# Optimization experiments

Measured on AMD Instinct MI355X. Metric: run time of the kernel, lower is better.

Reference implementation:

```python
import jax, jax.numpy as jnp
import numpy as np
import math

HID = 512
HEADS = 8
DK = HID // HEADS
B, S, T = 8, 4096, 512


def setup_inputs() -> dict:
    key = jax.random.key(0)
    ks = jax.random.split(key, 12)
    scale = 0.02
    inp = {
        "inputs": jax.random.normal(ks[0], (B, S, HID), dtype=jnp.float32),
        "targets": jax.random.normal(ks[1], (B, T, HID), dtype=jnp.float32),
        "mask": jnp.ones((B, S), dtype=bool),
        "Wq": jax.random.normal(ks[2], (HID, HID), dtype=jnp.float32) * scale,
        "bq": jnp.zeros((HID,), dtype=jnp.float32),
        "Wk": jax.random.normal(ks[3], (HID, HID), dtype=jnp.float32) * scale,
        "bk": jnp.zeros((HID,), dtype=jnp.float32),
        "Wv": jax.random.normal(ks[4], (HID, HID), dtype=jnp.float32) * scale,
        "bv": jnp.zeros((HID,), dtype=jnp.float32),
        "Wo": jax.random.normal(ks[5], (HID, HID), dtype=jnp.float32) * scale,
        "bo": jnp.zeros((HID,), dtype=jnp.float32),
    }
    return inp


def reference(inputs, targets, mask, Wq, bq, Wk, bk, Wv, bv, Wo, bo):
    # PoolingFunction(method='multihead-attention'), dropout=0 (identity),
    # hidden_size == output_size so mapping_function is identity.
    b, t, h = targets.shape
    s = inputs.shape[1]
    Q = (targets @ Wq.T + bq).reshape(b, t, HEADS, DK)
    K = (inputs @ Wk.T + bk).reshape(b, s, HEADS, DK)
    V = (inputs @ Wv.T + bv).reshape(b, s, HEADS, DK)
    # scores: b x heads x tgt x seq (same math as (Q*K).sum(-1)/sqrt(d_k))
    e = jnp.einsum('bthd,bshd->bhts', Q, K) / math.sqrt(DK)
    neg = (1.0 - mask.astype(jnp.float32)) * -1e20  # b x s
    e = e + neg[:, None, None, :]
    a = jax.nn.softmax(e, axis=-1)  # softmax over seq dim
    ctx = jnp.einsum('bhts,bshd->bthd', a, V).reshape(b, t, h)
    return ctx @ Wo.T + bo
```

## Files before the change

kernel.cpp:

```cpp
#include <hip/hip_runtime.h>
#include <hip/hip_bf16.h>
#include <cstdint>
#include <cstddef>

#define HIDN   512
#define NHEADS 8
#define BATCH  8
#define SLEN   4096
#define TLEN   512
#define SSPLIT 4
#define SCHUNK (SLEN / SSPLIT)
#define SCL2   0.18033688f

typedef __attribute__((ext_vector_type(8))) short   bf16x8;
typedef __attribute__((ext_vector_type(4))) float   f32x4;
typedef unsigned short u16;
typedef unsigned int   u32;

__device__ __forceinline__ u32 pkbf(float a, float b) {
    __hip_bfloat162 h = __float22bfloat162_rn(float2{a, b});
    union { __hip_bfloat162 h; u32 u; } un; un.h = h; return un.u;
}
__device__ __forceinline__ u32 cvtpk(float a, float b) {
    u32 r;
    asm("v_cvt_pk_bf16_f32 %0, %1, %2" : "=v"(r) : "v"(a), "v"(b));
    return r;
}
__device__ __forceinline__ float fexp2(float x) {
    return __builtin_amdgcn_exp2f(x);
}
__device__ __forceinline__ void gload_lds16(const u16* g, u16* l) {
    __builtin_amdgcn_global_load_lds(
        (const __attribute__((address_space(1))) u32*)g,
        (__attribute__((address_space(3))) u32*)l, 16, 0, 0);
}

__global__ __launch_bounds__(256) void cvt_all(
    const float* __restrict__ X, const float* __restrict__ Tg,
    const float* __restrict__ Wq, const float* __restrict__ Wk,
    const float* __restrict__ Wv, const float* __restrict__ Wo,
    const int* __restrict__ mask,
    u16* __restrict__ Xc, u16* __restrict__ Tc, u16* __restrict__ Wc,
    float* __restrict__ negf)
{
    int i4 = blockIdx.x * 256 + threadIdx.x;
    if (i4 >= 4980736) {
        int off = i4 - 4980736;
        int4 mv = ((const int4*)mask)[off];
        float4 nv;
        nv.x = mv.x ? 0.f : -1e30f; nv.y = mv.y ? 0.f : -1e30f;
        nv.z = mv.z ? 0.f : -1e30f; nv.w = mv.w ? 0.f : -1e30f;
        ((float4*)negf)[off] = nv;
        return;
    }
    const float* s; u16* d; long off;
    if (i4 < 4194304)      { s = X;  d = Xc; off = i4; }
    else if (i4 < 4718592) { s = Tg; d = Tc; off = i4 - 4194304; }
    else {
        int wi = i4 - 4718592; int widx = wi >> 16;
        s = (widx == 0) ? Wq : (widx == 1) ? Wk : (widx == 2) ? Wv : Wo;
        d = Wc + widx * 262144; off = wi & 65535;
    }
    float4 v = *(const float4*)(s + off * 4);
    uint2 o; o.x = pkbf(v.x, v.y); o.y = pkbf(v.z, v.w);
    *(uint2*)(d + off * 4) = o;
}

template<int MODE, int SEQ>
__global__ __launch_bounds__(256)
void gemm_bf16(const u16* __restrict__ A, const u16* __restrict__ Bw,
               const float* __restrict__ bias, void* __restrict__ Yv)
{
    __shared__ u16 As[128 * 32];
    __shared__ u16 Bs[128 * 32];
    const int tid = threadIdx.x;
    const int lane = tid & 63, w = tid >> 6;
    const int m = lane & 15, qd = lane >> 4;
    const int wm = w >> 1, wn = w & 1;
    const int m0 = blockIdx.y * 128, n0 = blockIdx.x * 128;

    f32x4 acc[4][4];
#pragma unroll
    for (int i = 0; i < 4; ++i)
#pragma unroll
        for (int j = 0; j < 4; ++j) acc[i][j] = (f32x4){0.f, 0.f, 0.f, 0.f};

    for (int k0 = 0; k0 < HIDN; k0 += 32) {
#pragma unroll
        for (int r = 0; r < 2; ++r) {
            const int f = tid + r * 256;
            const int row = f >> 2, c8 = (f & 3) * 8;
            const int fb = f & ~63;
            gload_lds16(A  + (size_t)(m0 + row) * HIDN + k0 + c8, As + fb * 8);
            gload_lds16(Bw + (size_t)(n0 + row) * HIDN + k0 + c8, Bs + fb * 8);
        }
        __syncthreads();
        bf16x8 af[4], bf[4];
#pragma unroll
        for (int t = 0; t < 4; ++t) {
            af[t] = *(bf16x8*)&As[(64 * wm + 16 * t + m) * 32 + 8 * qd];
            bf[t] = *(bf16x8*)&Bs[(64 * wn + 16 * t + m) * 32 + 8 * qd];
        }
#pragma unroll
        for (int ti = 0; ti < 4; ++ti)
#pragma unroll
            for (int tj = 0; tj < 4; ++tj)
                acc[ti][tj] = __builtin_amdgcn_mfma_f32_16x16x32_bf16(
                    af[ti], bf[tj], acc[ti][tj], 0, 0, 0);
        __syncthreads();
    }

#pragma unroll
    for (int ti = 0; ti < 4; ++ti) {
        const int gr0 = m0 + 64 * wm + 16 * ti + 4 * qd;
#pragma unroll
        for (int tj = 0; tj < 4; ++tj) {
            const int gcol = n0 + 64 * wn + 16 * tj + m;
            const float bv = bias[gcol];
            if (MODE == 0) {
                float* Y = (float*)Yv;
#pragma unroll
                for (int i = 0; i < 4; ++i)
                    Y[(size_t)(gr0 + i) * HIDN + gcol] = acc[ti][tj][i] + bv;
            } else {
                u16* Y = (u16*)Yv;
                const int b = gr0 / SEQ, h = gcol >> 6, d = gcol & 63;
                const int r = gr0 & (SEQ - 1);
                uint2 o;
                o.x = pkbf(acc[ti][tj][0] + bv, acc[ti][tj][1] + bv);
                o.y = pkbf(acc[ti][tj][2] + bv, acc[ti][tj][3] + bv);
                *(uint2*)&Y[(((size_t)(b * 8 + h)) * 64 + d) * SEQ + r] = o;
            }
        }
    }
}

template<int SEQ>
__global__ __launch_bounds__(256)
void gemm_wxT(const u16* __restrict__ Wm, const u16* __restrict__ X,
              const float* __restrict__ bias, u16* __restrict__ Y)
{
    __shared__ u16 As[128 * 32];
    __shared__ u16 Bs[128 * 32];
    const int tid = threadIdx.x;
    const int lane = tid & 63, w = tid >> 6;
    const int m = lane & 15, qd = lane >> 4;
    const int wm = w >> 1, wn = w & 1;
    const int m0 = blockIdx.y * 128, n0 = blockIdx.x * 128;

    f32x4 acc[4][4];
#pragma unroll
    for (int i = 0; i < 4; ++i)
#pragma unroll
        for (int j = 0; j < 4; ++j) acc[i][j] = (f32x4){0.f, 0.f, 0.f, 0.f};

    for (int k0 = 0; k0 < HIDN; k0 += 32) {
#pragma unroll
        for (int r = 0; r < 2; ++r) {
            const int f = tid + r * 256;
            const int row = f >> 2, c8 = (f & 3) * 8;
            const int fb = f & ~63;
            gload_lds16(Wm + (size_t)(m0 + row) * HIDN + k0 + c8, As + fb * 8);
            gload_lds16(X  + (size_t)(n0 + row) * HIDN + k0 + c8, Bs + fb * 8);
        }
        __syncthreads();
        bf16x8 af[4], bf[4];
#pragma unroll
        for (int t = 0; t < 4; ++t) {
            af[t] = *(bf16x8*)&As[(64 * wm + 16 * t + m) * 32 + 8 * qd];
            bf[t] = *(bf16x8*)&Bs[(64 * wn + 16 * t + m) * 32 + 8 * qd];
        }
#pragma unroll
        for (int ti = 0; ti < 4; ++ti)
#pragma unroll
            for (int tj = 0; tj < 4; ++tj)
                acc[ti][tj] = __builtin_amdgcn_mfma_f32_16x16x32_bf16(
                    af[ti], bf[tj], acc[ti][tj], 0, 0, 0);
        __syncthreads();
    }

#pragma unroll
    for (int ti = 0; ti < 4; ++ti) {
        const int o = m0 + 64 * wm + 16 * ti + 4 * qd;
        const float4 bv = *(const float4*)&bias[o];
        const int h = o >> 6, d0 = o & 63;
#pragma unroll
        for (int tj = 0; tj < 4; ++tj) {
            const int n = n0 + 64 * wn + 16 * tj + m;
            const int b = n / SEQ, r = n & (SEQ - 1);
            uint2 pk;
            pk.x = pkbf(acc[ti][tj][0] + bv.x, acc[ti][tj][1] + bv.y);
            pk.y = pkbf(acc[ti][tj][2] + bv.z, acc[ti][tj][3] + bv.w);
            *(uint2*)&Y[(((size_t)(b * 8 + h)) * SEQ + r) * 64 + d0] = pk;
        }
    }
}

__global__ __launch_bounds__(256, 2)
void attn_part(const u16* __restrict__ Q, const u16* __restrict__ K,
               const u16* __restrict__ Vt, const float* __restrict__ negf,
               float* __restrict__ Opart, float* __restrict__ lpart)
{
    __shared__ char Psh[32768];
    __shared__ u16  KVl[2][8192];
    __shared__ float Ngl[1024];
    const int tid = threadIdx.x;
    const int lane = tid & 63, w = tid >> 6;
    const int m = lane & 15, qd = lane >> 4;
    const int ti = blockIdx.x, si = blockIdx.y, bh = blockIdx.z;
    const int b = bh >> 3;

    const u16* Qp = Q + ((size_t)bh * TLEN + ti * 256) * 64;
    const u16* Kp = K + (size_t)bh * SLEN * 64;
    const u16* Vp = Vt + (size_t)bh * 64 * SLEN;
    const float* np = negf + (size_t)b * SLEN;
    const int s_beg = si * SCHUNK;

    const int sr = tid >> 3;
    const int sg = ((tid & 7) ^ (sr & 7)) * 8;
    const u16* kgb = Kp + (size_t)s_beg * 64 + sr * 64 + sg;
    const u16* vgb = Vp + s_beg + (size_t)sr * SLEN + sg;
    u16* kd = &KVl[0][0]    + tid * 8;
    u16* vd = &KVl[0][4096] + tid * 8;

#define STAGE(cc, bb) do {                                                   \
        const u16* kg_ = kgb + (size_t)(cc) * 4096;                          \
        const u16* vg_ = vgb + (cc) * 64;                                    \
        u16* kd_ = kd + (bb) * 8192;                                         \
        u16* vd_ = vd + (bb) * 8192;                                         \
        gload_lds16(kg_,                     kd_);                           \
        gload_lds16(kg_ + 32 * 64,           kd_ + 2048);                    \
        gload_lds16(vg_,                     vd_);                           \
        gload_lds16(vg_ + (size_t)32 * SLEN, vd_ + 2048);                    \
    } while (0)

    const int wb = w * 8192 + m * 128;
    int waddr[4], ra0[2], ra1[2];
#pragma unroll
    for (int st = 0; st < 4; ++st) waddr[st] = wb + (((4 * st + qd) ^ m) << 3);
#pragma unroll
    for (int ks = 0; ks < 2; ++ks) {
        const int u0 = 8 * ks + 2 * qd;
        ra0[ks] = wb + (((u0) ^ m) << 3);
        ra1[ks] = wb + (((u0 + 1) ^ m) << 3);
    }
    const int x0 = ((qd    ) ^ (m & 7)) * 8;
    const int x1 = ((4 + qd) ^ (m & 7)) * 8;

    bf16x8 qf[4][2];
#pragma unroll
    for (int ts = 0; ts < 4; ++ts)
#pragma unroll
        for (int kh = 0; kh < 2; ++kh)
            qf[ts][kh] = *(const bf16x8*)(Qp + (64 * w + 16 * ts + m) * 64 +
                                          32 * kh + 8 * qd);

    f32x4 O[4][4];
#pragma unroll
    for (int ts = 0; ts < 4; ++ts)
#pragma unroll
        for (int dt = 0; dt < 4; ++dt) O[ts][dt] = (f32x4){0.f, 0.f, 0.f, 0.f};
    float lr[4] = {0.f, 0.f, 0.f, 0.f};

#define CHUNK(cc) do {                                                       \
        const u16* Kl = &KVl[(cc) & 1][0];                                   \
        const u16* Vl = &KVl[(cc) & 1][4096];                                \
        bf16x8 kf[4][2];                                                     \
        _Pragma("unroll")                                                    \
        for (int st = 0; st < 4; ++st) {                                     \
            kf[st][0] = *(const bf16x8*)&Kl[st * 1024 + m * 64 + x0];        \
            kf[st][1] = *(const bf16x8*)&Kl[st * 1024 + m * 64 + x1];        \
        }                                                                    \
        float4 ng[4];                                                        \
        _Pragma("unroll")                                                    \
        for (int st = 0; st < 4; ++st)                                       \
            ng[st] = *(const float4*)&Ngl[((cc) << 6) + (st << 4) + (qd << 2)]; \
        _Pragma("unroll")                                                    \
        for (int ts = 0; ts < 4; ++ts) {                                     \
            f32x4 S[4];                                                      \
            _Pragma("unroll")                                                \
            for (int st = 0; st < 4; ++st) {                                 \
                f32x4 cc2 = (f32x4){0.f, 0.f, 0.f, 0.f};                     \
                cc2 = __builtin_amdgcn_mfma_f32_16x16x32_bf16(               \
                          kf[st][0], qf[ts][0], cc2, 0, 0, 0);               \
                cc2 = __builtin_amdgcn_mfma_f32_16x16x32_bf16(               \
                          kf[st][1], qf[ts][1], cc2, 0, 0, 0);               \
                S[st] = cc2;                                                 \
            }                                                                \
            float ls = 0.f;                                                  \
            _Pragma("unroll")                                                \
            for (int st = 0; st < 4; ++st) {                                 \
                const float p0 = fexp2(fmaf(S[st][0], SCL2, ng[st].x));      \
                const float p1 = fexp2(fmaf(S[st][1], SCL2, ng[st].y));      \
                const float p2 = fexp2(fmaf(S[st][2], SCL2, ng[st].z));      \
                const float p3 = fexp2(fmaf(S[st][3], SCL2, ng[st].w));      \
                ls += (p0 + p1) + (p2 + p3);                                 \
                *(uint2*)&Psh[waddr[st] + ts * 2048] =                       \
                    make_uint2(cvtpk(p0, p1), cvtpk(p2, p3));                \
            }                                                                \
            lr[ts] += ls;                                                    \
        }                                                                    \
        bf16x8 vf[4][2];                                                     \
        _Pragma("unroll")                                                    \
        for (int dt = 0; dt < 4; ++dt) {                                     \
            vf[dt][0] = *(const bf16x8*)&Vl[dt * 1024 + m * 64 + x0];        \
            vf[dt][1] = *(const bf16x8*)&Vl[dt * 1024 + m * 64 + x1];        \
        }                                                                    \
        __builtin_amdgcn_s_setprio(1);                                       \
        _Pragma("unroll")                                                    \
        for (int ts = 0; ts < 4; ++ts) {                                     \
            _Pragma("unroll")                                                \
            for (int ks = 0; ks < 2; ++ks) {                                 \
                const uint2 r0 = *(uint2*)&Psh[ra0[ks] + ts * 2048];         \
                const uint2 r1 = *(uint2*)&Psh[ra1[ks] + ts * 2048];         \
                union { uint4 u; bf16x8 v; } bu;                             \
                bu.u = make_uint4(r0.x, r0.y, r1.x, r1.y);                   \
                O[ts][0] = __builtin_amdgcn_mfma_f32_16x16x32_bf16(          \
                               vf[0][ks], bu.v, O[ts][0], 0, 0, 0);          \
                O[ts][1] = __builtin_amdgcn_mfma_f32_16x16x32_bf16(          \
                               vf[1][ks], bu.v, O[ts][1], 0, 0, 0);          \
                O[ts][2] = __builtin_amdgcn_mfma_f32_16x16x32_bf16(          \
                               vf[2][ks], bu.v, O[ts][2], 0, 0, 0);          \
                O[ts][3] = __builtin_amdgcn_mfma_f32_16x16x32_bf16(          \
                               vf[3][ks], bu.v, O[ts][3], 0, 0, 0);          \
            }                                                                \
        }                                                                    \
        __builtin_amdgcn_s_setprio(0);                                       \
    } while (0)

    STAGE(0, 0);
    gload_lds16((const u16*)(np + s_beg) + (size_t)tid * 8,
                ((u16*)Ngl) + tid * 8);
#pragma unroll 1
    for (int c = 0; c < (SCHUNK / 64) - 1; ++c) {
        STAGE(c + 1, (c + 1) & 1);
        asm volatile("s_waitcnt vmcnt(4)" ::: "memory");
        __builtin_amdgcn_s_barrier();
        __builtin_amdgcn_sched_barrier(0);
        CHUNK(c);
        __builtin_amdgcn_s_barrier();
        __builtin_amdgcn_sched_barrier(0);
    }
    asm volatile("s_waitcnt vmcnt(0)" ::: "memory");
    __builtin_amdgcn_s_barrier();
    __builtin_amdgcn_sched_barrier(0);
    CHUNK((SCHUNK / 64) - 1);

#undef STAGE
#undef CHUNK

#pragma unroll
    for (int ts = 0; ts < 4; ++ts) {
        float l = lr[ts];
        l += __shfl_xor(l, 16, 64);
        l += __shfl_xor(l, 32, 64);
        const int t = ti * 256 + 64 * w + 16 * ts + m;
        float* Ob = Opart + (((size_t)(si * 64 + bh)) * 512 + t) * 64;
#pragma unroll
        for (int dt = 0; dt < 4; ++dt)
            *(f32x4*)&Ob[16 * dt + 4 * qd] = O[ts][dt];
        if (qd == 0)
            lpart[((size_t)(si * 64 + bh)) * 512 + t] = l;
    }
}

__global__ __launch_bounds__(256)
void attn_combine(const float* __restrict__ Opart, const float* __restrict__ lpart,
                  u16* __restrict__ ctx)
{
    const int gid = blockIdx.x * 256 + threadIdx.x;
    const int d4 = gid & 15, t = (gid >> 4) & 511, bh = gid >> 13;
    const int b = bh >> 3, h = bh & 7;
    float4 o = {0.f, 0.f, 0.f, 0.f}; float l = 0.f;
#pragma unroll
    for (int si = 0; si < SSPLIT; ++si) {
        const size_t base = ((size_t)(si * 64 + bh)) * 512 + t;
        l += lpart[base];
        const float4 v = *(const float4*)(Opart + base * 64 + d4 * 4);
        o.x += v.x; o.y += v.y; o.z += v.z; o.w += v.w;
    }
    const float r = 1.f / l;
    uint2 pk; pk.x = pkbf(o.x * r, o.y * r); pk.y = pkbf(o.z * r, o.w * r);
    *(uint2*)&ctx[((size_t)(b * 512 + t)) * 512 + h * 64 + d4 * 4] = pk;
}

extern "C" void kernel_launch(void* const* d_in, const int* in_sizes, int n_in,
                              void* d_out, int out_size, void* d_ws, size_t ws_size,
                              hipStream_t stream)
{
    const float* inputs  = (const float*)d_in[0];
    const float* targets = (const float*)d_in[1];
    const int*   mask    = (const int*)d_in[2];
    const float* Wq = (const float*)d_in[3];
    const float* bq = (const float*)d_in[4];
    const float* Wk = (const float*)d_in[5];
    const float* bk = (const float*)d_in[6];
    const float* Wv = (const float*)d_in[7];
    const float* bv = (const float*)d_in[8];
    const float* Wo = (const float*)d_in[9];
    const float* bo = (const float*)d_in[10];

    char* ws = (char*)d_ws;
    u16*   Xc    = (u16*)(ws);
    u16*   Tc    = (u16*)(ws + 33554432);
    u16*   Wc    = (u16*)(ws + 37748736);
    float* negf  = (float*)(ws + 39845888);
    u16*   Qws   = (u16*)(ws + 39976960);
    u16*   Kws   = (u16*)(ws + 44171264);
    u16*   Vtws  = (u16*)(ws + 77725696);
    u16*   Cws   = (u16*)(ws + 111280128);
    float* Opart = (float*)(ws + 115474432);
    float* lpart = (float*)(ws + 149028864);

    cvt_all<<<19488, 256, 0, stream>>>(inputs, targets, Wq, Wk, Wv, Wo, mask,
                                       Xc, Tc, Wc, negf);

    gemm_wxT<TLEN><<<dim3(32, 4),  256, 0, stream>>>(Wc,          Tc, bq, Qws);
    gemm_wxT<SLEN><<<dim3(256, 4), 256, 0, stream>>>(Wc + 262144, Xc, bk, Kws);
    gemm_bf16<2, SLEN><<<dim3(4, 256), 256, 0, stream>>>(Xc, Wc + 524288, bv, Vtws);

    attn_part<<<dim3(2, SSPLIT, 64), 256, 0, stream>>>(Qws, Kws, Vtws, negf,
                                                       Opart, lpart);
    attn_combine<<<2048, 256, 0, stream>>>(Opart, lpart, Cws);

    gemm_bf16<0, TLEN><<<dim3(4, 32), 256, 0, stream>>>(Cws, Wc + 786432, bo,
                                                        (float*)d_out);
}
```

Baseline: 274.4 us.

## Double-buffer GEMM LDS tiles with async prefetch and XOR swizzle

Both projection GEMM kernels now keep two LDS buffers per operand and issue global-to-LDS loads for the next k-slice before computing the current one, using vmcnt waits and barriers instead of a full sync after each load. The LDS column index is also XOR-swizzled by row to reduce bank conflicts on the fragment reads. The aim is to hide global load latency behind MFMA work. In exchange, LDS use doubles, which may lower occupancy, and the hand-placed waitcnt and barriers must be correct.

New measurement: 279.4 us. No clear change (+1.8%).

```diff
diff --git a/kernel.cpp b/kernel.cpp
--- a/kernel.cpp
+++ b/kernel.cpp
@@ -66,18 +66,70 @@
     *(uint2*)(d + off * 4) = o;
 }
 
+#define GEMM_PIPE_DECLS                                                      \
+    const int xg = (qd ^ (m & 3)) * 8;                                       \
+    const int f0 = tid, f1 = tid + 256;                                      \
+    const int r0r = f0 >> 2, r0c = ((f0 & 3) ^ (r0r & 3)) * 8;               \
+    const int r1r = f1 >> 2, r1c = ((f1 & 3) ^ (r1r & 3)) * 8;               \
+    const int r0b = (f0 & ~63) * 8, r1b = (f1 & ~63) * 8
+
+#define GSTAGE(Aptr, Bptr, k0, bb) do {                                      \
+        gload_lds16(Aptr + (size_t)(m0 + r0r) * HIDN + (k0) + r0c,           \
+                    &As[bb][0] + r0b);                                       \
+        gload_lds16(Bptr + (size_t)(n0 + r0r) * HIDN + (k0) + r0c,           \
+                    &Bs[bb][0] + r0b);                                       \
+        gload_lds16(Aptr + (size_t)(m0 + r1r) * HIDN + (k0) + r1c,           \
+                    &As[bb][0] + r1b);                                       \
+        gload_lds16(Bptr + (size_t)(n0 + r1r) * HIDN + (k0) + r1c,           \
+                    &Bs[bb][0] + r1b);                                       \
+    } while (0)
+
+#define GCOMP(bb) do {                                                       \
+        bf16x8 af[4], bf[4];                                                 \
+        _Pragma("unroll")                                                    \
+        for (int t = 0; t < 4; ++t) {                                        \
+            af[t] = *(bf16x8*)&As[bb][(64 * wm + 16 * t + m) * 32 + xg];     \
+            bf[t] = *(bf16x8*)&Bs[bb][(64 * wn + 16 * t + m) * 32 + xg];     \
+        }                                                                    \
+        _Pragma("unroll")                                                    \
+        for (int ti = 0; ti < 4; ++ti)                                       \
+            _Pragma("unroll")                                                \
+            for (int tj = 0; tj < 4; ++tj)                                   \
+                acc[ti][tj] = __builtin_amdgcn_mfma_f32_16x16x32_bf16(       \
+                    af[ti], bf[tj], acc[ti][tj], 0, 0, 0);                   \
+    } while (0)
+
+#define GEMM_PIPE_LOOP(Aptr, Bptr) do {                                      \
+        GSTAGE(Aptr, Bptr, 0, 0);                                            \
+        _Pragma("unroll 1")                                                  \
+        for (int c = 0; c < (HIDN / 32) - 1; ++c) {                          \
+            GSTAGE(Aptr, Bptr, (c + 1) * 32, (c + 1) & 1);                   \
+            asm volatile("s_waitcnt vmcnt(4)" ::: "memory");                 \
+            __builtin_amdgcn_s_barrier();                                    \
+            __builtin_amdgcn_sched_barrier(0);                               \
+            GCOMP(c & 1);                                                    \
+            __builtin_amdgcn_s_barrier();                                    \
+            __builtin_amdgcn_sched_barrier(0);                               \
+        }                                                                    \
+        asm volatile("s_waitcnt vmcnt(0)" ::: "memory");                     \
+        __builtin_amdgcn_s_barrier();                                        \
+        __builtin_amdgcn_sched_barrier(0);                                   \
+        GCOMP(((HIDN / 32) - 1) & 1);                                        \
+    } while (0)
+
 template<int MODE, int SEQ>
 __global__ __launch_bounds__(256)
 void gemm_bf16(const u16* __restrict__ A, const u16* __restrict__ Bw,
                const float* __restrict__ bias, void* __restrict__ Yv)
 {
-    __shared__ u16 As[128 * 32];
-    __shared__ u16 Bs[128 * 32];
+    __shared__ u16 As[2][128 * 32];
+    __shared__ u16 Bs[2][128 * 32];
     const int tid = threadIdx.x;
     const int lane = tid & 63, w = tid >> 6;
     const int m = lane & 15, qd = lane >> 4;
     const int wm = w >> 1, wn = w & 1;
     const int m0 = blockIdx.y * 128, n0 = blockIdx.x * 128;
+    GEMM_PIPE_DECLS;
 
     f32x4 acc[4][4];
 #pragma unroll
@@ -85,30 +137,7 @@
 #pragma unroll
         for (int j = 0; j < 4; ++j) acc[i][j] = (f32x4){0.f, 0.f, 0.f, 0.f};
 
-    for (int k0 = 0; k0 < HIDN; k0 += 32) {
-#pragma unroll
-        for (int r = 0; r < 2; ++r) {
-            const int f = tid + r * 256;
-            const int row = f >> 2, c8 = (f & 3) * 8;
-            const int fb = f & ~63;
-            gload_lds16(A  + (size_t)(m0 + row) * HIDN + k0 + c8, As + fb * 8);
-            gload_lds16(Bw + (size_t)(n0 + row) * HIDN + k0 + c8, Bs + fb * 8);
-        }
-        __syncthreads();
-        bf16x8 af[4], bf[4];
-#pragma unroll
-        for (int t = 0; t < 4; ++t) {
-            af[t] = *(bf16x8*)&As[(64 * wm + 16 * t + m) * 32 + 8 * qd];
-            bf[t] = *(bf16x8*)&Bs[(64 * wn + 16 * t + m) * 32 + 8 * qd];
-        }
-#pragma unroll
-        for (int ti = 0; ti < 4; ++ti)
-#pragma unroll
-            for (int tj = 0; tj < 4; ++tj)
-                acc[ti][tj] = __builtin_amdgcn_mfma_f32_16x16x32_bf16(
-                    af[ti], bf[tj], acc[ti][tj], 0, 0, 0);
-        __syncthreads();
-    }
+    GEMM_PIPE_LOOP(A, Bw);
 
 #pragma unroll
     for (int ti = 0; ti < 4; ++ti) {
@@ -140,13 +169,14 @@
 void gemm_wxT(const u16* __restrict__ Wm, const u16* __restrict__ X,
               const float* __restrict__ bias, u16* __restrict__ Y)
 {
-    __shared__ u16 As[128 * 32];
-    __shared__ u16 Bs[128 * 32];
+    __shared__ u16 As[2][128 * 32];
+    __shared__ u16 Bs[2][128 * 32];
     const int tid = threadIdx.x;
     const int lane = tid & 63, w = tid >> 6;
     const int m = lane & 15, qd = lane >> 4;
     const int wm = w >> 1, wn = w & 1;
     const int m0 = blockIdx.y * 128, n0 = blockIdx.x * 128;
+    GEMM_PIPE_DECLS;
 
     f32x4 acc[4][4];
 #pragma unroll
@@ -154,30 +184,7 @@
 #pragma unroll
         for (int j = 0; j < 4; ++j) acc[i][j] = (f32x4){0.f, 0.f, 0.f, 0.f};
 
-    for (int k0 = 0; k0 < HIDN; k0 += 32) {
-#pragma unroll
-        for (int r = 0; r < 2; ++r) {
-            const int f = tid + r * 256;
-            const int row = f >> 2, c8 = (f & 3) * 8;
-            const int fb = f & ~63;
-            gload_lds16(Wm + (size_t)(m0 + row) * HIDN + k0 + c8, As + fb * 8);
-            gload_lds16(X  + (size_t)(n0 + row) * HIDN + k0 + c8, Bs + fb * 8);
-        }
-        __syncthreads();
-        bf16x8 af[4], bf[4];
-#pragma unroll
-        for (int t = 0; t < 4; ++t) {
-            af[t] = *(bf16x8*)&As[(64 * wm + 16 * t + m) * 32 + 8 * qd];
-            bf[t] = *(bf16x8*)&Bs[(64 * wn + 16 * t + m) * 32 + 8 * qd];
-        }
-#pragma unroll
-        for (int ti = 0; ti < 4; ++ti)
-#pragma unroll
-            for (int tj = 0; tj < 4; ++tj)
-                acc[ti][tj] = __builtin_amdgcn_mfma_f32_16x16x32_bf16(
-                    af[ti], bf[tj], acc[ti][tj], 0, 0, 0);
-        __syncthreads();
-    }
+    GEMM_PIPE_LOOP(Wm, X);
 
 #pragma unroll
     for (int ti = 0; ti < 4; ++ti) {
```
